# Optimization experiments

Measured on AMD Instinct MI355X. Metric: run time of the kernel, lower is better.

Reference implementation:

```python
import jax, jax.numpy as jnp
import numpy as np

B, CIN, COUT, H, W = 8, 128, 128, 64, 64
KH = KW = 3
STRIDE = PAD = 1
DIL = 1
K = KH * KW
EPS = 1e-4


def setup_inputs() -> dict:
    key = jax.random.key(0)
    k1, k2, k3 = jax.random.split(key, 3)
    Ho = (H + 2 * PAD - DIL * (KH - 1) - 1) // STRIDE + 1
    Wo = (W + 2 * PAD - DIL * (KW - 1) - 1) // STRIDE + 1
    x = jax.random.normal(k1, (B, CIN, H, W), dtype=jnp.float32)
    offset = jax.random.normal(k2, (B, 2 * K, Ho, Wo), dtype=jnp.float32)
    weight = jax.random.normal(k3, (COUT, CIN, KH, KW), dtype=jnp.float32) * 0.05
    return {"x": x, "offset": offset, "weight": weight}


def _bilinear_gather(x, py, px):
    # x: [B, C, H, W]; py/px: [B, K, Ho, Wo] float sampling positions
    Bn, C, Hn, Wn = x.shape
    x_flat = x.reshape(Bn, C, Hn * Wn)
    y0 = jnp.floor(py)
    x0 = jnp.floor(px)
    ly = py - y0  # fractional parts
    lx = px - x0
    out = 0.0
    corners = [(0.0, 0.0, (1 - ly) * (1 - lx)), (0.0, 1.0, (1 - ly) * lx),
               (1.0, 0.0, ly * (1 - lx)), (1.0, 1.0, ly * lx)]
    for dy, dx, wgt in corners:
        yy = y0 + dy
        xx = x0 + dx
        valid = (yy >= 0) & (yy < Hn) & (xx >= 0) & (xx < Wn)
        yi = jnp.clip(yy, 0, Hn - 1).astype(jnp.int32)
        xi = jnp.clip(xx, 0, Wn - 1).astype(jnp.int32)
        idx = (yi * Wn + xi).reshape(Bn, -1)  # [B, K*Ho*Wo]
        g = jax.vmap(lambda xf, ib: jnp.take(xf, ib, axis=1))(x_flat, idx)  # [B, C, N]
        out = out + g * (wgt * valid.astype(x.dtype)).reshape(Bn, 1, -1)
    return out  # [B, C, K*Ho*Wo]


def reference(x, offset, weight) -> jnp.ndarray:
    Bn = x.shape[0]
    Ho, Wo = offset.shape[2], offset.shape[3]
    # --- weight normalization (per output channel, per kernel tap) ---
    norm_fac = (KH * KW) ** 0.5
    length = jnp.sqrt(jnp.sum(jnp.square(weight) + EPS, axis=1, keepdims=True))  # [O,1,kh,kw]
    wn = weight / length / norm_fac  # [O, Cin, kh, kw]
    # --- sampling positions ---
    off = offset.reshape(Bn, K, 2, Ho, Wo)
    off_y, off_x = off[:, :, 0], off[:, :, 1]
    ky, kx = jnp.meshgrid(jnp.arange(KH), jnp.arange(KW), indexing="ij")
    ky = (ky.reshape(K) * DIL).astype(jnp.float32)
    kx = (kx.reshape(K) * DIL).astype(jnp.float32)
    base_y = (jnp.arange(Ho) * STRIDE - PAD).astype(jnp.float32)
    base_x = (jnp.arange(Wo) * STRIDE - PAD).astype(jnp.float32)
    py = base_y[None, None, :, None] + ky[None, :, None, None] + off_y  # [B,K,Ho,Wo]
    px = base_x[None, None, None, :] + kx[None, :, None, None] + off_x
    # --- deformable im2col + GEMM ---
    cols = _bilinear_gather(x, py, px).reshape(Bn, CIN, K, Ho, Wo)
    out = jnp.einsum("bckhw,ock->bohw", cols, wn.reshape(COUT, CIN, K))
    return out
```

## Files before the change

### kernel.cpp

```cpp
#include <hip/hip_runtime.h>
#include <hip/hip_bf16.h>
#include <hip/hip_fp16.h>
#include <math.h>


typedef __attribute__((ext_vector_type(8))) short short8;
typedef __attribute__((ext_vector_type(4))) float floatx4;
typedef __attribute__((ext_vector_type(2))) float floatx2;

static __device__ __forceinline__ unsigned int f2bf(float f) {
    unsigned int u = __float_as_uint(f);
    u += 0x7fffu + ((u >> 16) & 1u);
    return u >> 16;
}
static __device__ __forceinline__ unsigned int packbf2(float lo, float hi) {
    __hip_bfloat162 h = __float22bfloat162_rn(make_float2(lo, hi));
    unsigned int u;
    __builtin_memcpy(&u, &h, 4);
    return u;
}
static __device__ __forceinline__ floatx2 bf2f2(unsigned int w) {
    floatx2 r;
    r.x = __uint_as_float(w << 16);
    r.y = __uint_as_float(w & 0xffff0000u);
    return r;
}

__global__ void prep_k(const float* __restrict__ x, const float* __restrict__ w,
                       unsigned int* __restrict__ xt32, unsigned short* __restrict__ wb) {
    __shared__ float lds[128 * 65];
    const int tid = threadIdx.x;

    if (blockIdx.x < 512) {
        const int b = blockIdx.x & 7, h = (blockIdx.x >> 3) & 63;
        const float* xp = x + (b * 128 * 64 + h) * 64;
        #pragma unroll 4
        for (int i = 0; i < 32; i++) {
            const int c = i * 4 + (tid >> 6);
            const int ww = tid & 63;
            lds[c * 65 + ww] = xp[c * 4096 + ww];
        }
        __syncthreads();
        unsigned int* xo = xt32 + (b * 64 + h) * 4096;
        #pragma unroll 4
        for (int i = 0; i < 16; i++) {
            const int flat2 = i * 256 + tid;
            const int ww = flat2 >> 6, cp = flat2 & 63;
            xo[flat2] = packbf2(lds[(2 * cp) * 65 + ww], lds[(2 * cp + 1) * 65 + ww]);
        }
    } else {
        const int o = (blockIdx.x - 512) * 4 + (tid >> 6);
        const int lane = tid & 63;
        const float* wo = w + o * 1152;
        float v[18];
        #pragma unroll
        for (int i = 0; i < 18; i++) v[i] = wo[lane * 18 + i];
        float s[9];
        #pragma unroll
        for (int k = 0; k < 9; k++) s[k] = v[k] * v[k] + v[9 + k] * v[9 + k];
        #pragma unroll
        for (int d = 32; d >= 1; d >>= 1) {
            #pragma unroll
            for (int k = 0; k < 9; k++) s[k] += __shfl_xor(s[k], d, 64);
        }
        const int c0 = 2 * lane, c1 = c0 + 1;
        #pragma unroll
        for (int k = 0; k < 9; k++) {
            const float inv = 1.0f / (3.0f * sqrtf(s[k] + 0.0128f));
            wb[((k * 16 + (c0 >> 3)) * 128 + o) * 8 + (c0 & 7)] = (unsigned short)f2bf(v[k] * inv);
            wb[((k * 16 + (c1 >> 3)) * 128 + o) * 8 + (c1 & 7)] = (unsigned short)f2bf(v[9 + k] * inv);
        }
    }
}

static __device__ __forceinline__ unsigned int bl1(const float4 w,
                                                   unsigned int r0, unsigned int r1,
                                                   unsigned int r2, unsigned int r3) {
    floatx2 a = bf2f2(r0) * w.x;
    a += bf2f2(r1) * w.y;
    a += bf2f2(r2) * w.z;
    a += bf2f2(r3) * w.w;
    return packbf2(a.x, a.y);
}

static __device__ __forceinline__ uint4 combine4(const float4 wvv,
                                                 const uint4 r0, const uint4 r1,
                                                 const uint4 r2, const uint4 r3) {
    uint4 pk;
    pk.x = bl1(wvv, r0.x, r1.x, r2.x, r3.x);
    pk.y = bl1(wvv, r0.y, r1.y, r2.y, r3.y);
    pk.z = bl1(wvv, r0.z, r1.z, r2.z, r3.z);
    pk.w = bl1(wvv, r0.w, r1.w, r2.w, r3.w);
    return pk;
}

__global__ __launch_bounds__(512, 4) void dconv_k(
    const unsigned short* __restrict__ xt, const float* __restrict__ off,
    const unsigned short* __restrict__ wb, float* __restrict__ out)
{
    __shared__ alignas(16) float4 tapW[576];
    __shared__ alignas(16) int4  tapI[576];
    __shared__ alignas(16) unsigned short colsS[2][16 * 520];

    const int idx = blockIdx.x;
    const int b = idx & 7;
    const int ho = (idx >> 3) & 63;
    const int tid = threadIdx.x;

    for (int t = tid; t < 576; t += 512) {
        const int k = t >> 6, p = t & 63;
        const int oidx = ((b * 18 + 2 * k) * 64 + ho) * 64 + p;
        const float offy = off[oidx];
        const float offx = off[oidx + 4096];
        const float py = (float)(ho - 1 + (k / 3)) + offy;
        const float px = (float)(p - 1 + (k % 3)) + offx;
        const float y0f = floorf(py), x0f = floorf(px);
        const float ly = py - y0f, lx = px - x0f;
        const int y0 = (int)y0f, x0 = (int)x0f;
        const int y1 = y0 + 1, x1 = x0 + 1;
        const float fy0 = (y0 >= 0 && y0 < 64) ? (1.0f - ly) : 0.0f;
        const float fy1 = (y1 >= 0 && y1 < 64) ? ly : 0.0f;
        const float fx0 = (x0 >= 0 && x0 < 64) ? (1.0f - lx) : 0.0f;
        const float fx1 = (x1 >= 0 && x1 < 64) ? lx : 0.0f;
        const int yc0 = min(max(y0, 0), 63), yc1 = min(max(y1, 0), 63);
        const int xc0 = min(max(x0, 0), 63), xc1 = min(max(x1, 0), 63);
        tapW[t] = make_float4(fy0 * fx0, fy0 * fx1, fy1 * fx0, fy1 * fx1);
        tapI[t] = make_int4((yc0 * 64 + xc0) << 7, (yc0 * 64 + xc1) << 7,
                            (yc1 * 64 + xc0) << 7, (yc1 * 64 + xc1) << 7);
    }
    __syncthreads();

    const int lane = tid & 63, wv = tid >> 6;
    const int quad = lane >> 4, l16 = lane & 15;
    const int g = tid & 15, p0 = tid >> 4;
    const unsigned short* xb = xt + b * (64 * 64 * 128);
    const int obase = wv * 16;

    floatx4 acc[4];
    #pragma unroll
    for (int t = 0; t < 4; t++) acc[t] = (floatx4)0.0f;

    #pragma unroll
    for (int i = 0; i < 2; i++) {
        const int p = p0 + i * 32;
        const float4 wvv = tapW[p];
        const int4 iv = tapI[p];
        const uint4 r0 = *(const uint4*)(xb + iv.x + g * 8);
        const uint4 r1 = *(const uint4*)(xb + iv.y + g * 8);
        const uint4 r2 = *(const uint4*)(xb + iv.z + g * 8);
        const uint4 r3 = *(const uint4*)(xb + iv.w + g * 8);
        *(uint4*)&colsS[0][g * 520 + p * 8] = combine4(wvv, r0, r1, r2, r3);
    }
    __syncthreads();

    for (int k = 0; k < 9; k++) {
        const int cur = k & 1;

        const unsigned short* wk = wb + k * 16384;
        short8 a[4];
        #pragma unroll
        for (int q = 0; q < 4; q++) {
            const int cgrp = q * 4 + quad;
            a[q] = *(const short8*)(wk + (cgrp * 128 + obase + l16) * 8);
        }

        uint4 r[2][4];
        float4 wvv[2]; int4 ivd[2];
        if (k < 8) {
            #pragma unroll
            for (int i = 0; i < 2; i++) {
                const int p = p0 + i * 32;
                wvv[i] = tapW[(k + 1) * 64 + p];
                ivd[i] = tapI[(k + 1) * 64 + p];
                r[i][0] = *(const uint4*)(xb + ivd[i].x + g * 8);
                r[i][1] = *(const uint4*)(xb + ivd[i].y + g * 8);
                r[i][2] = *(const uint4*)(xb + ivd[i].z + g * 8);
                r[i][3] = *(const uint4*)(xb + ivd[i].w + g * 8);
            }
        }

        #pragma unroll
        for (int q = 0; q < 4; q++) {
            const int cgrp = q * 4 + quad;
            #pragma unroll
            for (int t = 0; t < 4; t++) {
                const short8 bf = *(const short8*)&colsS[cur][cgrp * 520 + (t * 16 + l16) * 8];
                acc[t] = __builtin_amdgcn_mfma_f32_16x16x32_bf16(a[q], bf, acc[t], 0, 0, 0);
            }
        }

        if (k < 8) {
            #pragma unroll
            for (int i = 0; i < 2; i++) {
                const int p = p0 + i * 32;
                *(uint4*)&colsS[cur ^ 1][g * 520 + p * 8] =
                    combine4(wvv[i], r[i][0], r[i][1], r[i][2], r[i][3]);
            }
            __syncthreads();
        }
    }

    float* ob = out + b * 128 * 4096 + ho * 64;
    #pragma unroll
    for (int t = 0; t < 4; t++) {
        const int pix = t * 16 + l16;
        #pragma unroll
        for (int r2 = 0; r2 < 4; r2++) {
            __builtin_nontemporal_store(acc[t][r2],
                &ob[(obase + quad * 4 + r2) * 4096 + pix]);
        }
    }
}

extern "C" void kernel_launch(void* const* d_in, const int* in_sizes, int n_in,
                              void* d_out, int out_size, void* d_ws, size_t ws_size,
                              hipStream_t stream) {
    const float* x   = (const float*)d_in[0];
    const float* off = (const float*)d_in[1];
    const float* w   = (const float*)d_in[2];
    float* out = (float*)d_out;

    unsigned short* xt = (unsigned short*)d_ws;
    unsigned short* wbuf = xt + 8 * 64 * 64 * 128;

    hipLaunchKernelGGL(prep_k,  dim3(544), dim3(256), 0, stream,
                       x, w, (unsigned int*)xt, wbuf);
    hipLaunchKernelGGL(dconv_k, dim3(512), dim3(512), 0, stream, xt, off, wbuf, out);
}
```

Baseline: 98.35 us.

## Pack tap records into fp16/u16 and retile waves to 32x32 output blocks

Tap bilinear weights are now stored as fp16 and corner indices as 16-bit values in a single uint4 record, halving shared memory for the tap table and the LDS reads per tap. Each wave now computes a 32-output-channel by 32-pixel tile instead of 16 channels by 64 pixels, so every loaded B fragment from LDS feeds two MFMAs and LDS reads per MFMA drop. The cost is twice as many weight fragment loads from global memory per wave, extra unpack instructions, and reduced precision for the bilinear weights.

```diff
diff --git a/kernel.cpp b/kernel.cpp
--- a/kernel.cpp
+++ b/kernel.cpp
@@ -94,12 +94,19 @@
     return pk;
 }
 
+static __device__ __forceinline__ void rec_expand(const uint4 rec, float4& wvv, int4& iv) {
+    const float2 w01 = __half22float2(*reinterpret_cast<const __half2*>(&rec.x));
+    const float2 w23 = __half22float2(*reinterpret_cast<const __half2*>(&rec.y));
+    wvv = make_float4(w01.x, w01.y, w23.x, w23.y);
+    iv = make_int4((int)(rec.z & 0xffffu) << 7, (int)(rec.z >> 16) << 7,
+                   (int)(rec.w & 0xffffu) << 7, (int)(rec.w >> 16) << 7);
+}
+
 __global__ __launch_bounds__(512, 4) void dconv_k(
     const unsigned short* __restrict__ xt, const float* __restrict__ off,
     const unsigned short* __restrict__ wb, float* __restrict__ out)
 {
-    __shared__ alignas(16) float4 tapW[576];
-    __shared__ alignas(16) int4  tapI[576];
+    __shared__ alignas(16) uint4 tapG[576];
     __shared__ alignas(16) unsigned short colsS[2][16 * 520];
 
     const int idx = blockIdx.x;
@@ -124,9 +131,14 @@
         const float fx1 = (x1 >= 0 && x1 < 64) ? lx : 0.0f;
         const int yc0 = min(max(y0, 0), 63), yc1 = min(max(y1, 0), 63);
         const int xc0 = min(max(x0, 0), 63), xc1 = min(max(x1, 0), 63);
-        tapW[t] = make_float4(fy0 * fx0, fy0 * fx1, fy1 * fx0, fy1 * fx1);
-        tapI[t] = make_int4((yc0 * 64 + xc0) << 7, (yc0 * 64 + xc1) << 7,
-                            (yc1 * 64 + xc0) << 7, (yc1 * 64 + xc1) << 7);
+        const __half2 a01 = __float22half2_rn(make_float2(fy0 * fx0, fy0 * fx1));
+        const __half2 a23 = __float22half2_rn(make_float2(fy1 * fx0, fy1 * fx1));
+        uint4 pk;
+        __builtin_memcpy(&pk.x, &a01, 4);
+        __builtin_memcpy(&pk.y, &a23, 4);
+        pk.z = (unsigned int)(yc0 * 64 + xc0) | ((unsigned int)(yc0 * 64 + xc1) << 16);
+        pk.w = (unsigned int)(yc1 * 64 + xc0) | ((unsigned int)(yc1 * 64 + xc1) << 16);
+        tapG[t] = pk;
     }
     __syncthreads();
 
@@ -134,7 +146,9 @@
     const int quad = lane >> 4, l16 = lane & 15;
     const int g = tid & 15, p0 = tid >> 4;
     const unsigned short* xb = xt + b * (64 * 64 * 128);
-    const int obase = wv * 16;
+    const int ph = wv & 1,  cq = wv >> 1;
+    const int pbase = ph * 32;
+    const int obase = cq * 32;
 
     floatx4 acc[4];
     #pragma unroll
@@ -143,8 +157,8 @@
     #pragma unroll
     for (int i = 0; i < 2; i++) {
         const int p = p0 + i * 32;
-        const float4 wvv = tapW[p];
-        const int4 iv = tapI[p];
+        float4 wvv; int4 iv;
+        rec_expand(tapG[p], wvv, iv);
         const uint4 r0 = *(const uint4*)(xb + iv.x + g * 8);
         const uint4 r1 = *(const uint4*)(xb + iv.y + g * 8);
         const uint4 r2 = *(const uint4*)(xb + iv.z + g * 8);
@@ -157,36 +171,39 @@
         const int cur = k & 1;
 
         const unsigned short* wk = wb + k * 16384;
-        short8 a[4];
+        short8 a[8];
         #pragma unroll
         for (int q = 0; q < 4; q++) {
             const int cgrp = q * 4 + quad;
-            a[q] = *(const short8*)(wk + (cgrp * 128 + obase + l16) * 8);
+            #pragma unroll
+            for (int n = 0; n < 2; n++)
+                a[q * 2 + n] = *(const short8*)(wk + (cgrp * 128 + obase + n * 16 + l16) * 8);
         }
 
         uint4 r[2][4];
-        float4 wvv[2]; int4 ivd[2];
+        float4 wvv[2];
         if (k < 8) {
             #pragma unroll
             for (int i = 0; i < 2; i++) {
                 const int p = p0 + i * 32;
-                wvv[i] = tapW[(k + 1) * 64 + p];
-                ivd[i] = tapI[(k + 1) * 64 + p];
-                r[i][0] = *(const uint4*)(xb + ivd[i].x + g * 8);
-                r[i][1] = *(const uint4*)(xb + ivd[i].y + g * 8);
-                r[i][2] = *(const uint4*)(xb + ivd[i].z + g * 8);
-                r[i][3] = *(const uint4*)(xb + ivd[i].w + g * 8);
+                int4 iv;
+                rec_expand(tapG[(k + 1) * 64 + p], wvv[i], iv);
+                r[i][0] = *(const uint4*)(xb + iv.x + g * 8);
+                r[i][1] = *(const uint4*)(xb + iv.y + g * 8);
+                r[i][2] = *(const uint4*)(xb + iv.z + g * 8);
+                r[i][3] = *(const uint4*)(xb + iv.w + g * 8);
             }
         }
 
         #pragma unroll
         for (int q = 0; q < 4; q++) {
             const int cgrp = q * 4 + quad;
-            #pragma unroll
-            for (int t = 0; t < 4; t++) {
-                const short8 bf = *(const short8*)&colsS[cur][cgrp * 520 + (t * 16 + l16) * 8];
-                acc[t] = __builtin_amdgcn_mfma_f32_16x16x32_bf16(a[q], bf, acc[t], 0, 0, 0);
-            }
+            const short8 bf0 = *(const short8*)&colsS[cur][cgrp * 520 + (pbase + l16) * 8];
+            const short8 bf1 = *(const short8*)&colsS[cur][cgrp * 520 + (pbase + 16 + l16) * 8];
+            acc[0] = __builtin_amdgcn_mfma_f32_16x16x32_bf16(a[q * 2 + 0], bf0, acc[0], 0, 0, 0);
+            acc[1] = __builtin_amdgcn_mfma_f32_16x16x32_bf16(a[q * 2 + 1], bf0, acc[1], 0, 0, 0);
+            acc[2] = __builtin_amdgcn_mfma_f32_16x16x32_bf16(a[q * 2 + 0], bf1, acc[2], 0, 0, 0);
+            acc[3] = __builtin_amdgcn_mfma_f32_16x16x32_bf16(a[q * 2 + 1], bf1, acc[3], 0, 0, 0);
         }
 
         if (k < 8) {
@@ -202,12 +219,15 @@
 
     float* ob = out + b * 128 * 4096 + ho * 64;
     #pragma unroll
-    for (int t = 0; t < 4; t++) {
-        const int pix = t * 16 + l16;
-        #pragma unroll
-        for (int r2 = 0; r2 < 4; r2++) {
-            __builtin_nontemporal_store(acc[t][r2],
-                &ob[(obase + quad * 4 + r2) * 4096 + pix]);
+    for (int t = 0; t < 2; t++) {
+        const int pix = pbase + t * 16 + l16;
+        #pragma unroll
+        for (int n = 0; n < 2; n++) {
+            #pragma unroll
+            for (int r2 = 0; r2 < 4; r2++) {
+                __builtin_nontemporal_store(acc[t * 2 + n][r2],
+                    &ob[(obase + n * 16 + quad * 4 + r2) * 4096 + pix]);
+            }
         }
     }
 }
```

Measured after the change: 101.4 us. 3.1% more time.
